# Kernel tuning notes

Measured on AMD Instinct MI355X. Metric: run time of the kernel, lower is better.

## Reference

```python
import jax, jax.numpy as jnp
import numpy as np

B, C, H, W = 2, 512, 64, 64
G = 32  # GroupNorm groups
EPS = 1e-6


def setup_inputs() -> dict:
    key = jax.random.key(0)
    ks = jax.random.split(key, 6)
    s = 1.0 / np.sqrt(C)
    return {
        "x": jax.random.normal(ks[0], (B, C, H, W), dtype=jnp.float32),
        "gn_w": jnp.ones((C,), dtype=jnp.float32),
        "gn_b": jnp.zeros((C,), dtype=jnp.float32),
        "wq": jax.random.normal(ks[1], (C, C), dtype=jnp.float32) * s,
        "bq": jnp.zeros((C,), dtype=jnp.float32),
        "wk": jax.random.normal(ks[2], (C, C), dtype=jnp.float32) * s,
        "bk": jnp.zeros((C,), dtype=jnp.float32),
        "wv": jax.random.normal(ks[3], (C, C), dtype=jnp.float32) * s,
        "bv": jnp.zeros((C,), dtype=jnp.float32),
        "wo": jax.random.normal(ks[4], (C, C), dtype=jnp.float32) * s,
        "bo": jnp.zeros((C,), dtype=jnp.float32),
    }


def _group_norm(x, w, b):
    b_, c_, h_, w_ = x.shape
    xg = x.reshape(b_, G, c_ // G, h_ * w_)
    mu = jnp.mean(xg, axis=(2, 3), keepdims=True)
    var = jnp.var(xg, axis=(2, 3), keepdims=True)
    xn = (xg - mu) * jax.lax.rsqrt(var + EPS)
    xn = xn.reshape(b_, c_, h_ * w_)
    return xn * w[None, :, None] + b[None, :, None]  # [B, C, N]


def reference(x, gn_w, gn_b, wq, bq, wk, bk, wv, bv, wo, bo):
    b, c, h, w = x.shape
    hn = _group_norm(x, gn_w, gn_b)  # [B, C, N]
    # 1x1 convs == per-pixel matmuls over channel dim
    q = jnp.einsum('oc,bcn->bon', wq, hn) + bq[None, :, None]
    k = jnp.einsum('oc,bcn->bon', wk, hn) + bk[None, :, None]
    v = jnp.einsum('oc,bcn->bon', wv, hn) + bv[None, :, None]
    scale = jnp.asarray(c, x.dtype) ** -0.5
    attn = jnp.einsum('bci,bcj->bij', q, k) * scale  # [B, N, N]
    attn = jax.nn.softmax(attn, axis=-1)
    o = jnp.einsum('bij,bcj->bci', attn, v)  # [B, C, N]
    o = jnp.einsum('oc,bcn->bon', wo, o) + bo[None, :, None]
    return x + o.reshape(b, c, h, w)
```

## Files before the change

kernel.cpp:

```cpp
#include <hip/hip_runtime.h>

#define CC 512
#define NPIX 4096
#define NB 2
#define NG 32
#define GSIZE 16
#define EPS 1e-6f

typedef unsigned short u16;
typedef __bf16 bf16x8 __attribute__((ext_vector_type(8)));
typedef float f32x4 __attribute__((ext_vector_type(4)));

__device__ __forceinline__ float bf2f(u16 u) {
  union { unsigned int i; float f; } c; c.i = ((unsigned int)u) << 16; return c.f;
}
__device__ __forceinline__ u16 f2bf(float f) {
  union { float f; unsigned int i; } c; c.f = f;
  unsigned int u = c.i;
  return (u16)((u + 0x7fffu + ((u >> 16) & 1u)) >> 16);
}

__global__ __launch_bounds__(256) void f2bf4x4_kernel(
    const float* __restrict__ s0, const float* __restrict__ s1,
    const float* __restrict__ s2, const float* __restrict__ s3,
    u16* __restrict__ d0, u16* __restrict__ d1,
    u16* __restrict__ d2, u16* __restrict__ d3) {
  const float* s; u16* d;
  switch (blockIdx.y) {
    case 0: s = s0; d = d0; break;
    case 1: s = s1; d = d1; break;
    case 2: s = s2; d = d2; break;
    default: s = s3; d = d3; break;
  }
  int i = blockIdx.x * 256 + threadIdx.x;
  float4 v = ((const float4*)s)[i];
  uint2 pk;
  pk.x = (unsigned)f2bf(v.x) | ((unsigned)f2bf(v.y) << 16);
  pk.y = (unsigned)f2bf(v.z) | ((unsigned)f2bf(v.w) << 16);
  ((uint2*)d)[i] = pk;
}

__global__ __launch_bounds__(256) void concat2_kernel(const float* __restrict__ a,
                                                      const float* __restrict__ b,
                                                      float* __restrict__ o) {
  int i = blockIdx.x * 256 + threadIdx.x;
  o[i] = (i < CC) ? a[i] : b[i - CC];
}

__global__ __launch_bounds__(256) void gn_stats_kernel(const float* __restrict__ x,
                                                       float* __restrict__ stats) {
  int bg = blockIdx.x;
  const float4* p = (const float4*)(x + (long)bg * (GSIZE * NPIX));
  float s = 0.f, ss = 0.f;
  for (int i = threadIdx.x; i < GSIZE * NPIX / 4; i += 256) {
    float4 v = p[i];
    s  += v.x + v.y + v.z + v.w;
    ss += v.x * v.x + v.y * v.y + v.z * v.z + v.w * v.w;
  }
  for (int off = 32; off; off >>= 1) { s += __shfl_xor(s, off); ss += __shfl_xor(ss, off); }
  __shared__ float rs[4], rss[4];
  int wid = threadIdx.x >> 6;
  if ((threadIdx.x & 63) == 0) { rs[wid] = s; rss[wid] = ss; }
  __syncthreads();
  if (threadIdx.x == 0) {
    s = rs[0] + rs[1] + rs[2] + rs[3];
    ss = rss[0] + rss[1] + rss[2] + rss[3];
    float mean = s / (float)(GSIZE * NPIX);
    float var = ss / (float)(GSIZE * NPIX) - mean * mean;
    stats[bg * 2] = mean;
    stats[bg * 2 + 1] = rsqrtf(var + EPS);
  }
}

__global__ __launch_bounds__(256) void gn_apply_kernel(const float* __restrict__ x,
                                                       const float* __restrict__ stats,
                                                       const float* __restrict__ gw,
                                                       const float* __restrict__ gb,
                                                       u16* __restrict__ hn) {
  int n0 = blockIdx.x * 64, c0 = blockIdx.y * 64, b = blockIdx.z;
  __shared__ float tile[64][65];
  int t = threadIdx.x;
  int nj = t & 63, cw = t >> 6;
  #pragma unroll
  for (int r = 0; r < 16; ++r) {
    int ci = cw * 16 + r;
    int c = c0 + ci;
    float mean = stats[(b * NG + (c >> 4)) * 2];
    float rstd = stats[(b * NG + (c >> 4)) * 2 + 1];
    float v = x[((long)b * CC + c) * NPIX + n0 + nj];
    tile[ci][nj] = (v - mean) * rstd * gw[c] + gb[c];
  }
  __syncthreads();
  #pragma unroll
  for (int r = 0; r < 16; ++r) {
    int nn = cw * 16 + r;
    hn[((long)b * NPIX + n0 + nn) * CC + c0 + nj] = f2bf(tile[nj][nn]);
  }
}

__global__ __launch_bounds__(256) void lred_kernel(const float* __restrict__ Lp,
                                                   float* __restrict__ L) {
  int i = blockIdx.x * 256 + threadIdx.x;
  int bz = i / NPIX, row = i % NPIX;
  float s = 0.f;
  #pragma unroll
  for (int b = 0; b < 16; ++b) s += Lp[((long)bz * 16 + b) * NPIX + row];
  L[i] = s;
}

#define BM 128
#define BN 128
#define BKT 64
#define BUFSZ 8192

template<int OUTF32, int BIASMODE, int RESID, int EPI>
__global__ __launch_bounds__(256) void gemm_nt(
    const u16* __restrict__ A, int lda, long aBatch,
    const u16* __restrict__ B, int ldb, long bBatch,
    void* __restrict__ C, int ldc, long cBatch,
    const float* __restrict__ bias,
    const float* __restrict__ resid, long rBatch,
    float* __restrict__ L, int lOff,
    int K, float scale) {
  __shared__ u16 SH[2 * 2 * BUFSZ];
  const int t = threadIdx.x;

  int nwgx = gridDim.x, nwgy = gridDim.y;
  int flat = blockIdx.x + nwgx * (blockIdx.y + nwgy * blockIdx.z);
  int nwg = nwgx * nwgy * gridDim.z;
  int newflat = (flat % 8) * (nwg / 8) + flat / 8;
  const int bx = newflat % nwgx;
  int tmpf = newflat / nwgx;
  const int by = tmpf % nwgy;
  const int bz = tmpf / nwgy;

  const int m0 = by * BM;
  const int n0 = bx * BN;
  const u16* Ab = A + (long)bz * aBatch;
  const u16* Bb = B + (long)bz * bBatch;

  const int lane = t & 63;
  const int wid = t >> 6;
  const int wr = (wid >> 1) * 64;
  const int wc = (wid & 1) * 64;
  const int r16 = lane & 15;
  const int q = lane >> 4;

  const int sRow = wid * 8 + (lane >> 3);
  const int sCol = (((lane & 7) ^ (lane >> 3)) * 8);

  f32x4 acc[4][4] = {};
  const int rsw = r16 & 7;

  const int nt = K / BKT;

  auto stage = [&](int c, int k0) {
    u16* aDst = SH + c * 2 * BUFSZ + wid * 512;
    u16* bDst = SH + c * 2 * BUFSZ + BUFSZ + wid * 512;
    #pragma unroll
    for (int p = 0; p < 4; ++p) {
      __builtin_amdgcn_global_load_lds(
          (const __attribute__((address_space(1))) unsigned int*)(Ab + (long)(m0 + p * 32 + sRow) * lda + k0 + sCol),
          (__attribute__((address_space(3))) unsigned int*)(aDst + p * 2048),
          16, 0, 0);
      __builtin_amdgcn_global_load_lds(
          (const __attribute__((address_space(1))) unsigned int*)(Bb + (long)(n0 + p * 32 + sRow) * ldb + k0 + sCol),
          (__attribute__((address_space(3))) unsigned int*)(bDst + p * 2048),
          16, 0, 0);
    }
  };

  stage(0, 0);

  for (int tt = 0; tt < nt; ++tt) {
    const int pre = tt + 1;
    if (pre < nt) {
      stage(pre & 1, pre * BKT);
      asm volatile("s_waitcnt vmcnt(8)" ::: "memory");
    } else {
      asm volatile("s_waitcnt vmcnt(0)" ::: "memory");
    }
    __builtin_amdgcn_s_barrier();
    __builtin_amdgcn_sched_barrier(0);

    const u16* As_b = SH + (tt & 1) * 2 * BUFSZ;
    const u16* Bs_b = As_b + BUFSZ;
    #pragma unroll
    for (int kk = 0; kk < BKT; kk += 32) {
      bf16x8 af[4], bfr[4];
      const int c0q = (kk >> 3) + q;
      const int colSw = (c0q ^ rsw) * 8;
      #pragma unroll
      for (int i = 0; i < 4; ++i) {
        af[i]  = *(const bf16x8*)&As_b[(wr + i * 16 + r16) * BKT + colSw];
        bfr[i] = *(const bf16x8*)&Bs_b[(wc + i * 16 + r16) * BKT + colSw];
      }
      #pragma unroll
      for (int i = 0; i < 4; ++i)
        #pragma unroll
        for (int j = 0; j < 4; ++j)
          acc[i][j] = __builtin_amdgcn_mfma_f32_16x16x32_bf16(af[i], bfr[j], acc[i][j], 0, 0, 0);
    }
    __builtin_amdgcn_s_barrier();
    __builtin_amdgcn_sched_barrier(0);
  }

  if (EPI == 1) {
    #pragma unroll
    for (int i = 0; i < 4; ++i) {
      #pragma unroll
      for (int r = 0; r < 4; ++r) {
        int row = m0 + wr + i * 16 + q * 4 + r;
        float s = 0.f;
        #pragma unroll
        for (int j = 0; j < 4; ++j) {
          float p = __expf(acc[i][j][r] * scale);
          s += p;
          int col = n0 + wc + j * 16 + r16;
          ((u16*)C)[(long)bz * cBatch + (long)row * ldc + col] = f2bf(p);
        }
        s += __shfl_xor(s, 1); s += __shfl_xor(s, 2);
        s += __shfl_xor(s, 4); s += __shfl_xor(s, 8);
        if (r16 == 0) atomicAdd(&L[(long)bz * NPIX + lOff + row], s);
      }
    }
    return;
  }

  #pragma unroll
  for (int i = 0; i < 4; ++i) {
    #pragma unroll
    for (int r = 0; r < 4; ++r) {
      int row = m0 + wr + i * 16 + q * 4 + r;
      float inv = 1.0f;
      if (EPI == 2) inv = 1.0f / L[(long)bz * NPIX + lOff + row];
      #pragma unroll
      for (int j = 0; j < 4; ++j) {
        int col = n0 + wc + j * 16 + r16;
        float v = acc[i][j][r] * scale;
        if (EPI == 2) v *= inv;
        if (BIASMODE == 1) v += bias[row];
        if (BIASMODE == 2) v += bias[col];
        long off = (long)bz * cBatch + (long)row * ldc + col;
        if (RESID) v += resid[(long)bz * rBatch + (long)row * ldc + col];
        if (OUTF32) ((float*)C)[off] = v;
        else        ((u16*)C)[off] = f2bf(v);
      }
    }
  }
}

__global__ __launch_bounds__(512, 1) void gemm256_exp(
    const u16* __restrict__ A, int lda, long aBatch,
    const u16* __restrict__ B, int ldb, long bBatch,
    u16* __restrict__ C, int ldc, long cBatch,
    float* __restrict__ Lp,
    int K, float scale) {
  __shared__ u16 SH[2][32768];
  const int t = threadIdx.x;

  int nwgx = gridDim.x, nwgy = gridDim.y;
  int flat = blockIdx.x + nwgx * (blockIdx.y + nwgy * blockIdx.z);
  int nwg = nwgx * nwgy * gridDim.z;
  int newflat = (flat % 8) * (nwg / 8) + flat / 8;
  const int bx = newflat % nwgx;
  int tmpf = newflat / nwgx;
  const int by = tmpf % nwgy;
  const int bz = tmpf / nwgy;

  const int m0 = by * 256;
  const int n0 = bx * 256;
  const u16* Ab = A + (long)bz * aBatch;
  const u16* Bb = B + (long)bz * bBatch;
  u16* Cb = C + (long)bz * cBatch;

  const int lane = t & 63;
  const int wid = t >> 6;
  const int wrow = (wid >> 2) * 128;
  const int wcol = (wid & 3) * 64;
  const int r16 = lane & 15;
  const int q = lane >> 4;
  const int rsw = r16 & 7;

  const int sRow = t >> 3;
  const int sCol = ((t & 7) ^ ((t >> 3) & 7)) * 8;

  auto stage = [&](int d, int k0) {
    u16* base = &SH[d][0];
    #pragma unroll
    for (int i = 0; i < 4; ++i)
      __builtin_amdgcn_global_load_lds(
          (const __attribute__((address_space(1))) unsigned int*)(Ab + (long)(m0 + i * 64 + sRow) * lda + k0 + sCol),
          (__attribute__((address_space(3))) unsigned int*)(base + i * 4096 + wid * 512),
          16, 0, 0);
    #pragma unroll
    for (int i = 0; i < 4; ++i)
      __builtin_amdgcn_global_load_lds(
          (const __attribute__((address_space(1))) unsigned int*)(Bb + (long)(n0 + i * 64 + sRow) * ldb + k0 + sCol),
          (__attribute__((address_space(3))) unsigned int*)(base + 16384 + i * 4096 + wid * 512),
          16, 0, 0);
  };

  f32x4 acc[8][4] = {};
  const int nt = K / 64;

  stage(0, 0);

  for (int tt = 0; tt < nt; ++tt) {
    if (tt + 1 < nt) {
      stage((tt + 1) & 1, (tt + 1) * 64);
      asm volatile("s_waitcnt vmcnt(8)" ::: "memory");
    } else {
      asm volatile("s_waitcnt vmcnt(0)" ::: "memory");
    }
    __builtin_amdgcn_s_barrier();

    const u16* As_ = &SH[tt & 1][0];
    const u16* Bs_ = As_ + 16384;
    #pragma unroll
    for (int kk = 0; kk < 2; ++kk) {
      const int cs = ((kk * 4 + q) ^ rsw) * 8;
      bf16x8 af[8], bfv[4];
      #pragma unroll
      for (int i = 0; i < 8; ++i)
        af[i] = *(const bf16x8*)&As_[(wrow + i * 16 + r16) * 64 + cs];
      #pragma unroll
      for (int i = 0; i < 4; ++i)
        bfv[i] = *(const bf16x8*)&Bs_[(wcol + i * 16 + r16) * 64 + cs];
      #pragma unroll
      for (int mi = 0; mi < 8; ++mi)
        #pragma unroll
        for (int ni = 0; ni < 4; ++ni)
          acc[mi][ni] = __builtin_amdgcn_mfma_f32_16x16x32_bf16(af[mi], bfv[ni], acc[mi][ni], 0, 0, 0);
    }
    __builtin_amdgcn_s_barrier();
  }

  float* Lsh = (float*)&SH[0][0];
  #pragma unroll
  for (int mi = 0; mi < 8; ++mi) {
    #pragma unroll
    for (int r = 0; r < 4; ++r) {
      int lrow = mi * 16 + q * 4 + r;
      int row = m0 + wrow + lrow;
      float s = 0.f;
      #pragma unroll
      for (int ni = 0; ni < 4; ++ni) {
        float p = __expf(acc[mi][ni][r] * scale);
        s += p;
        Cb[(long)row * ldc + n0 + wcol + ni * 16 + r16] = f2bf(p);
      }
      s += __shfl_xor(s, 1); s += __shfl_xor(s, 2);
      s += __shfl_xor(s, 4); s += __shfl_xor(s, 8);
      if (r16 == 0) Lsh[((wrow >> 7) * 128 + lrow) * 4 + (wcol >> 6)] = s;
    }
  }
  __syncthreads();
  if (t < 256) {
    const float* lr = &Lsh[t * 4];
    Lp[((long)bz * 16 + bx) * NPIX + m0 + t] = lr[0] + lr[1] + lr[2] + lr[3];
  }
}

extern "C" void kernel_launch(void* const* d_in, const int* in_sizes, int n_in,
                              void* d_out, int out_size, void* d_ws, size_t ws_size,
                              hipStream_t stream) {
  const float* x   = (const float*)d_in[0];
  const float* gnw = (const float*)d_in[1];
  const float* gnb = (const float*)d_in[2];
  const float* wq  = (const float*)d_in[3];
  const float* bq  = (const float*)d_in[4];
  const float* wk  = (const float*)d_in[5];
  const float* bk_ = (const float*)d_in[6];
  const float* wv  = (const float*)d_in[7];
  const float* bv  = (const float*)d_in[8];
  const float* wo  = (const float*)d_in[9];
  const float* bo  = (const float*)d_in[10];
  float* out = (float*)d_out;

  char* wsp = (char*)d_ws;
  auto alloc = [&](size_t bytes) {
    char* r = wsp; wsp += (bytes + 255) & ~(size_t)255; return r;
  };
  u16* wqb = (u16*)alloc((size_t)CC * CC * 2);
  u16* wkb = (u16*)alloc((size_t)CC * CC * 2);
  u16* wvb = (u16*)alloc((size_t)CC * CC * 2);
  u16* wob = (u16*)alloc((size_t)CC * CC * 2);
  float* bqk = (float*)alloc((size_t)2 * CC * 4);
  float* stats = (float*)alloc((size_t)NB * NG * 2 * 4);
  float* lsum = (float*)alloc((size_t)NB * NPIX * 4);
  float* lpart = (float*)alloc((size_t)NB * 16 * NPIX * 4);
  u16* hn  = (u16*)alloc((size_t)NB * NPIX * CC * 2);
  u16* qkt = (u16*)alloc((size_t)NB * NPIX * (2 * CC) * 2);
  u16* vcn = (u16*)alloc((size_t)NB * CC * NPIX * 2);
  u16* ot  = (u16*)alloc((size_t)NB * NPIX * CC * 2);
  size_t used = (size_t)(wsp - (char*)d_ws);
  size_t rem = ws_size > used ? ws_size - used : 0;
  int CH = 256;
  if ((size_t)NB * 1024 * NPIX * 2 <= rem) CH = 1024;
  if ((size_t)NB * 4096 * NPIX * 2 <= rem) CH = 4096;
  u16* SP = (u16*)alloc((size_t)NB * CH * NPIX * 2);

  dim3 blk(256);
  f2bf4x4_kernel<<<dim3(CC * CC / 1024, 4), blk, 0, stream>>>(
      wq, wk, wv, wo, wqb, wkb, wvb, wob);
  concat2_kernel<<<2 * CC / 256, blk, 0, stream>>>(bq, bk_, bqk);
  hipMemsetAsync(lsum, 0, (size_t)NB * NPIX * 4, stream);

  gn_stats_kernel<<<NB * NG, blk, 0, stream>>>(x, stats);
  gn_apply_kernel<<<dim3(NPIX / 64, CC / 64, NB), blk, 0, stream>>>(x, stats, gnw, gnb, hn);

  gemm_nt<0, 2, 0, 0><<<dim3(2 * CC / BN, NPIX / BM, NB), blk, 0, stream>>>(
      hn, CC, (long)NPIX * CC, wqb, CC, 0, qkt, 2 * CC, (long)NPIX * 2 * CC,
      bqk, nullptr, 0, nullptr, 0, CC, 1.0f);
  gemm_nt<0, 1, 0, 0><<<dim3(NPIX / BN, CC / BM, NB), blk, 0, stream>>>(
      wvb, CC, 0, hn, CC, (long)NPIX * CC, vcn, NPIX, (long)CC * NPIX,
      bv, nullptr, 0, nullptr, 0, CC, 1.0f);

  const u16* qt = qkt;
  const u16* kt = qkt + CC;
  const float scale = 0.044194173824159216f;
  for (int i0 = 0; i0 < NPIX; i0 += CH) {
    if (CH == 4096) {
      gemm256_exp<<<dim3(NPIX / 256, NPIX / 256, NB), dim3(512), 0, stream>>>(
          qt, 2 * CC, (long)NPIX * 2 * CC, kt, 2 * CC, (long)NPIX * 2 * CC,
          SP, NPIX, (long)CH * NPIX, lpart, CC, scale);
      lred_kernel<<<NB * NPIX / 256, blk, 0, stream>>>(lpart, lsum);
    } else {
      gemm_nt<0, 0, 0, 1><<<dim3(NPIX / BN, CH / BM, NB), blk, 0, stream>>>(
          qt + (long)i0 * 2 * CC, 2 * CC, (long)NPIX * 2 * CC, kt, 2 * CC, (long)NPIX * 2 * CC,
          SP, NPIX, (long)CH * NPIX, nullptr, nullptr, 0, lsum, i0, CC, scale);
    }
    gemm_nt<0, 0, 0, 2><<<dim3(CC / BN, CH / BM, NB), blk, 0, stream>>>(
        SP, NPIX, (long)CH * NPIX, vcn, NPIX, (long)CC * NPIX,
        ot + (long)i0 * CC, CC, (long)NPIX * CC, nullptr, nullptr, 0, lsum, i0, NPIX, 1.0f);
  }

  gemm_nt<1, 1, 1, 0><<<dim3(NPIX / BN, CC / BM, NB), blk, 0, stream>>>(
      wob, CC, 0, ot, CC, (long)NPIX * CC, out, NPIX, (long)CC * NPIX,
      bo, x, (long)CC * NPIX, nullptr, 0, CC, 1.0f);
}
```

Before: 166.0 us.

## Triple-buffer QK^T exp GEMM with K=32 tiles and interleaved prefetch

Reworks the gemm256_exp main loop from a double-buffered K=64 tile to a triple-buffered K=32 tile with a prefetch distance of two. Global-to-LDS loads for the tile two steps ahead are split into halves and issued between LDS fragment reads and MFMA bursts. Priority raising is added around the MFMA blocks. The aim is to hide global load latency and LDS waits behind matrix work. In exchange there are more loop iterations and barriers, a new swizzle pattern for the narrower tile, and tighter vmcnt accounting that must match the number of loads in flight.

```diff
diff --git a/kernel.cpp b/kernel.cpp
--- a/kernel.cpp
+++ b/kernel.cpp
@@ -250,13 +250,16 @@
   }
 }
 
+#define BK3 32
+#define TBUF 8192
+
 __global__ __launch_bounds__(512, 1) void gemm256_exp(
     const u16* __restrict__ A, int lda, long aBatch,
     const u16* __restrict__ B, int ldb, long bBatch,
     u16* __restrict__ C, int ldc, long cBatch,
     float* __restrict__ Lp,
     int K, float scale) {
-  __shared__ u16 SH[2][32768];
+  __shared__ u16 SH[3][2 * TBUF];
   const int t = threadIdx.x;
 
   int nwgx = gridDim.x, nwgy = gridDim.y;
@@ -280,62 +283,79 @@
   const int wcol = (wid & 3) * 64;
   const int r16 = lane & 15;
   const int q = lane >> 4;
-  const int rsw = r16 & 7;
-
-  const int sRow = t >> 3;
-  const int sCol = ((t & 7) ^ ((t >> 3) & 7)) * 8;
-
-  auto stage = [&](int d, int k0) {
-    u16* base = &SH[d][0];
-    #pragma unroll
-    for (int i = 0; i < 4; ++i)
-      __builtin_amdgcn_global_load_lds(
-          (const __attribute__((address_space(1))) unsigned int*)(Ab + (long)(m0 + i * 64 + sRow) * lda + k0 + sCol),
-          (__attribute__((address_space(3))) unsigned int*)(base + i * 4096 + wid * 512),
-          16, 0, 0);
-    #pragma unroll
-    for (int i = 0; i < 4; ++i)
-      __builtin_amdgcn_global_load_lds(
-          (const __attribute__((address_space(1))) unsigned int*)(Bb + (long)(n0 + i * 64 + sRow) * ldb + k0 + sCol),
-          (__attribute__((address_space(3))) unsigned int*)(base + 16384 + i * 4096 + wid * 512),
-          16, 0, 0);
+
+  const int sRow = t >> 2;
+  const int sCol = ((t & 3) ^ ((t >> 3) & 3)) * 8;
+
+  auto stageHalf = [&](int buf, int k0, int op, int half) {
+    const u16* src = (op ? Bb + (long)(n0 + half * 128 + sRow) * ldb
+                         : Ab + (long)(m0 + half * 128 + sRow) * lda) + k0 + sCol;
+    u16* dst = &SH[buf][op * TBUF + half * 4096 + wid * 512];
+    __builtin_amdgcn_global_load_lds(
+        (const __attribute__((address_space(1))) unsigned int*)src,
+        (__attribute__((address_space(3))) unsigned int*)dst, 16, 0, 0);
   };
+  auto stageTile = [&](int buf, int k0) {
+    stageHalf(buf, k0, 0, 0); stageHalf(buf, k0, 1, 0);
+    stageHalf(buf, k0, 0, 1); stageHalf(buf, k0, 1, 1);
+  };
 
   f32x4 acc[8][4] = {};
-  const int nt = K / 64;
-
-  stage(0, 0);
+  const int nt = K / BK3;
+  const int cs = (q ^ ((r16 >> 1) & 3)) * 8;
+
+  stageTile(0, 0);
+  stageTile(1, BK3);
 
   for (int tt = 0; tt < nt; ++tt) {
     if (tt + 1 < nt) {
-      stage((tt + 1) & 1, (tt + 1) * 64);
-      asm volatile("s_waitcnt vmcnt(8)" ::: "memory");
+      asm volatile("s_waitcnt vmcnt(4)" ::: "memory");
     } else {
       asm volatile("s_waitcnt vmcnt(0)" ::: "memory");
     }
     __builtin_amdgcn_s_barrier();
-
-    const u16* As_ = &SH[tt & 1][0];
-    const u16* Bs_ = As_ + 16384;
-    #pragma unroll
-    for (int kk = 0; kk < 2; ++kk) {
-      const int cs = ((kk * 4 + q) ^ rsw) * 8;
-      bf16x8 af[8], bfv[4];
-      #pragma unroll
-      for (int i = 0; i < 8; ++i)
-        af[i] = *(const bf16x8*)&As_[(wrow + i * 16 + r16) * 64 + cs];
-      #pragma unroll
-      for (int i = 0; i < 4; ++i)
-        bfv[i] = *(const bf16x8*)&Bs_[(wcol + i * 16 + r16) * 64 + cs];
-      #pragma unroll
-      for (int mi = 0; mi < 8; ++mi)
-        #pragma unroll
-        for (int ni = 0; ni < 4; ++ni)
-          acc[mi][ni] = __builtin_amdgcn_mfma_f32_16x16x32_bf16(af[mi], bfv[ni], acc[mi][ni], 0, 0, 0);
-    }
+    __builtin_amdgcn_sched_barrier(0);
+
+    const u16* As_ = &SH[tt % 3][0];
+    const u16* Bs_ = As_ + TBUF;
+    const int pre = tt + 2;
+
+    bf16x8 a1[4], bfv[4];
+    #pragma unroll
+    for (int i = 0; i < 4; ++i)
+      a1[i] = *(const bf16x8*)&As_[(wrow + i * 16 + r16) * BK3 + cs];
+    #pragma unroll
+    for (int i = 0; i < 4; ++i)
+      bfv[i] = *(const bf16x8*)&Bs_[(wcol + i * 16 + r16) * BK3 + cs];
+    if (pre < nt) { stageHalf(pre % 3, pre * BK3, 0, 0); stageHalf(pre % 3, pre * BK3, 1, 0); }
+    asm volatile("s_waitcnt lgkmcnt(0)" ::: "memory");
+    __builtin_amdgcn_sched_barrier(0);
+    __builtin_amdgcn_s_setprio(1);
+    #pragma unroll
+    for (int mi = 0; mi < 4; ++mi)
+      #pragma unroll
+      for (int ni = 0; ni < 4; ++ni)
+        acc[mi][ni] = __builtin_amdgcn_mfma_f32_16x16x32_bf16(a1[mi], bfv[ni], acc[mi][ni], 0, 0, 0);
+    __builtin_amdgcn_s_setprio(0);
     __builtin_amdgcn_s_barrier();
-  }
-
+
+    bf16x8 a2[4];
+    #pragma unroll
+    for (int i = 0; i < 4; ++i)
+      a2[i] = *(const bf16x8*)&As_[(wrow + (4 + i) * 16 + r16) * BK3 + cs];
+    if (pre < nt) { stageHalf(pre % 3, pre * BK3, 0, 1); stageHalf(pre % 3, pre * BK3, 1, 1); }
+    asm volatile("s_waitcnt lgkmcnt(0)" ::: "memory");
+    __builtin_amdgcn_sched_barrier(0);
+    __builtin_amdgcn_s_setprio(1);
+    #pragma unroll
+    for (int mi = 0; mi < 4; ++mi)
+      #pragma unroll
+      for (int ni = 0; ni < 4; ++ni)
+        acc[4 + mi][ni] = __builtin_amdgcn_mfma_f32_16x16x32_bf16(a2[mi], bfv[ni], acc[4 + mi][ni], 0, 0, 0);
+    __builtin_amdgcn_s_setprio(0);
+  }
+
+  __builtin_amdgcn_s_barrier();
   float* Lsh = (float*)&SH[0][0];
   #pragma unroll
   for (int mi = 0; mi < 8; ++mi) {
```

New measurement: 170.8 us. 1.03x slower.

## Fold Wq^T·Wk and Wo·Wv into combined weights to drop projection GEMMs

Applied to the files above, without the earlier changes.

Precomputes Wq^T·Wk and Wo·Wv as bf16 matrices with a small batched GEMM. The score GEMM then uses hn directly against hn·(Wq^T Wk), and the PV GEMM writes the final output with softmax normalisation, folded bias and residual in a new epilogue. The bk term is dropped because it is constant along each softmax row, and the bq contribution becomes a per-key column bias added inside the exp. This removes the Q projection and the output-projection GEMM plus the ot intermediate, at the cost of small transpose, weight-product and bias kernels, and extra bf16 rounding from the precomposed weights.

```diff
diff --git a/kernel.cpp b/kernel.cpp
--- a/kernel.cpp
+++ b/kernel.cpp
@@ -20,18 +20,8 @@
   return (u16)((u + 0x7fffu + ((u >> 16) & 1u)) >> 16);
 }
 
-__global__ __launch_bounds__(256) void f2bf4x4_kernel(
-    const float* __restrict__ s0, const float* __restrict__ s1,
-    const float* __restrict__ s2, const float* __restrict__ s3,
-    u16* __restrict__ d0, u16* __restrict__ d1,
-    u16* __restrict__ d2, u16* __restrict__ d3) {
-  const float* s; u16* d;
-  switch (blockIdx.y) {
-    case 0: s = s0; d = d0; break;
-    case 1: s = s1; d = d1; break;
-    case 2: s = s2; d = d2; break;
-    default: s = s3; d = d3; break;
-  }
+__global__ __launch_bounds__(256) void f2bf1_kernel(const float* __restrict__ s,
+                                                    u16* __restrict__ d) {
   int i = blockIdx.x * 256 + threadIdx.x;
   float4 v = ((const float4*)s)[i];
   uint2 pk;
@@ -40,11 +30,74 @@
   ((uint2*)d)[i] = pk;
 }
 
-__global__ __launch_bounds__(256) void concat2_kernel(const float* __restrict__ a,
-                                                      const float* __restrict__ b,
-                                                      float* __restrict__ o) {
+__global__ __launch_bounds__(256) void f2bfT_kernel(
+    const float* __restrict__ s0, const float* __restrict__ s1,
+    const float* __restrict__ s2,
+    u16* __restrict__ d0, u16* __restrict__ d1, u16* __restrict__ d2) {
+  const float* s; u16* d;
+  switch (blockIdx.z) {
+    case 0: s = s0; d = d0; break;
+    case 1: s = s1; d = d1; break;
+    default: s = s2; d = d2; break;
+  }
+  __shared__ float tile[64][65];
+  int a0 = blockIdx.x * 64, b0 = blockIdx.y * 64;
+  int tx = threadIdx.x & 63, w = threadIdx.x >> 6;
+  #pragma unroll
+  for (int r = 0; r < 16; ++r) {
+    int row = w * 16 + r;
+    tile[row][tx] = s[(long)(b0 + row) * CC + a0 + tx];
+  }
+  __syncthreads();
+  #pragma unroll
+  for (int r = 0; r < 16; ++r) {
+    int row = w * 16 + r;
+    d[(long)(a0 + row) * CC + b0 + tx] = f2bf(tile[tx][row]);
+  }
+}
+
+__global__ __launch_bounds__(256) void ubias_kernel(const u16* __restrict__ wkT,
+                                                    const float* __restrict__ bq,
+                                                    float* __restrict__ u) {
+  int b = blockIdx.x * 256 + threadIdx.x;
+  const u16* row = wkT + (long)b * CC;
+  float s = 0.f;
+  for (int c = 0; c < CC; c += 8) {
+    uint4 raw = *(const uint4*)(row + c);
+    const u16* pr = (const u16*)&raw;
+    #pragma unroll
+    for (int k = 0; k < 8; ++k) s += bf2f(pr[k]) * bq[c + k];
+  }
+  u[b] = s;
+}
+
+__global__ __launch_bounds__(256) void wobv_kernel(const float* __restrict__ wo,
+                                                   const float* __restrict__ bv,
+                                                   const float* __restrict__ bo,
+                                                   float* __restrict__ wobv) {
+  int o = blockIdx.x * 256 + threadIdx.x;
+  const float* row = wo + (long)o * CC;
+  float s = bo[o];
+  for (int c = 0; c < CC; c += 4) {
+    float4 v = *(const float4*)(row + c);
+    s += v.x * bv[c] + v.y * bv[c + 1] + v.z * bv[c + 2] + v.w * bv[c + 3];
+  }
+  wobv[o] = s;
+}
+
+__global__ __launch_bounds__(256) void cb_kernel(const u16* __restrict__ hn,
+                                                 const float* __restrict__ u,
+                                                 float* __restrict__ cb, float scale) {
   int i = blockIdx.x * 256 + threadIdx.x;
-  o[i] = (i < CC) ? a[i] : b[i - CC];
+  const u16* row = hn + (long)i * CC;
+  float s = 0.f;
+  for (int c = 0; c < CC; c += 8) {
+    uint4 raw = *(const uint4*)(row + c);
+    const u16* pr = (const u16*)&raw;
+    #pragma unroll
+    for (int k = 0; k < 8; ++k) s += bf2f(pr[k]) * u[c + k];
+  }
+  cb[i] = s * scale;
 }
 
 __global__ __launch_bounds__(256) void gn_stats_kernel(const float* __restrict__ x,
@@ -121,6 +174,7 @@
     const float* __restrict__ bias,
     const float* __restrict__ resid, long rBatch,
     float* __restrict__ L, int lOff,
+    const float* __restrict__ cbias,
     int K, float scale) {
   __shared__ u16 SH[2 * 2 * BUFSZ];
   const int t = threadIdx.x;
@@ -206,6 +260,10 @@
   }
 
   if (EPI == 1) {
+    float cbv[4];
+    #pragma unroll
+    for (int j = 0; j < 4; ++j)
+      cbv[j] = cbias[(long)bz * NPIX + n0 + wc + j * 16 + r16];
     #pragma unroll
     for (int i = 0; i < 4; ++i) {
       #pragma unroll
@@ -214,7 +272,7 @@
         float s = 0.f;
         #pragma unroll
         for (int j = 0; j < 4; ++j) {
-          float p = __expf(acc[i][j][r] * scale);
+          float p = __expf(acc[i][j][r] * scale + cbv[j]);
           s += p;
           int col = n0 + wc + j * 16 + r16;
           ((u16*)C)[(long)bz * cBatch + (long)row * ldc + col] = f2bf(p);
@@ -227,18 +285,38 @@
     return;
   }
 
+  if (EPI == 3) {
+    float invc[4];
+    #pragma unroll
+    for (int j = 0; j < 4; ++j)
+      invc[j] = 1.0f / L[(long)bz * NPIX + lOff + n0 + wc + j * 16 + r16];
+    #pragma unroll
+    for (int i = 0; i < 4; ++i) {
+      #pragma unroll
+      for (int r = 0; r < 4; ++r) {
+        int row = m0 + wr + i * 16 + q * 4 + r;
+        float bia = bias[row];
+        #pragma unroll
+        for (int j = 0; j < 4; ++j) {
+          int col = n0 + wc + j * 16 + r16;
+          long off = (long)bz * cBatch + (long)row * ldc + col;
+          ((float*)C)[off] = acc[i][j][r] * invc[j] + bia +
+                             resid[(long)bz * rBatch + (long)row * ldc + col];
+        }
+      }
+    }
+    return;
+  }
+
   #pragma unroll
   for (int i = 0; i < 4; ++i) {
     #pragma unroll
     for (int r = 0; r < 4; ++r) {
       int row = m0 + wr + i * 16 + q * 4 + r;
-      float inv = 1.0f;
-      if (EPI == 2) inv = 1.0f / L[(long)bz * NPIX + lOff + row];
       #pragma unroll
       for (int j = 0; j < 4; ++j) {
         int col = n0 + wc + j * 16 + r16;
         float v = acc[i][j][r] * scale;
-        if (EPI == 2) v *= inv;
         if (BIASMODE == 1) v += bias[row];
         if (BIASMODE == 2) v += bias[col];
         long off = (long)bz * cBatch + (long)row * ldc + col;
@@ -254,7 +332,7 @@
     const u16* __restrict__ A, int lda, long aBatch,
     const u16* __restrict__ B, int ldb, long bBatch,
     u16* __restrict__ C, int ldc, long cBatch,
-    float* __restrict__ Lp,
+    float* __restrict__ Lp, const float* __restrict__ cb,
     int K, float scale) {
   __shared__ u16 SH[2][32768];
   const int t = threadIdx.x;
@@ -336,6 +414,10 @@
     __builtin_amdgcn_s_barrier();
   }
 
+  float cbv[4];
+  #pragma unroll
+  for (int ni = 0; ni < 4; ++ni)
+    cbv[ni] = cb[(long)bz * NPIX + n0 + wcol + ni * 16 + r16];
   float* Lsh = (float*)&SH[0][0];
   #pragma unroll
   for (int mi = 0; mi < 8; ++mi) {
@@ -346,7 +428,7 @@
       float s = 0.f;
       #pragma unroll
       for (int ni = 0; ni < 4; ++ni) {
-        float p = __expf(acc[mi][ni][r] * scale);
+        float p = __expf(acc[mi][ni][r] * scale + cbv[ni]);
         s += p;
         Cb[(long)row * ldc + n0 + wcol + ni * 16 + r16] = f2bf(p);
       }
@@ -377,23 +459,25 @@
   const float* wo  = (const float*)d_in[9];
   const float* bo  = (const float*)d_in[10];
   float* out = (float*)d_out;
+  (void)bk_;
 
   char* wsp = (char*)d_ws;
   auto alloc = [&](size_t bytes) {
     char* r = wsp; wsp += (bytes + 255) & ~(size_t)255; return r;
   };
-  u16* wqb = (u16*)alloc((size_t)CC * CC * 2);
-  u16* wkb = (u16*)alloc((size_t)CC * CC * 2);
-  u16* wvb = (u16*)alloc((size_t)CC * CC * 2);
-  u16* wob = (u16*)alloc((size_t)CC * CC * 2);
-  float* bqk = (float*)alloc((size_t)2 * CC * 4);
+  const size_t WSZ = (size_t)CC * CC;
+  u16* wA = (u16*)alloc(2 * WSZ * 2);
+  u16* wB = (u16*)alloc(2 * WSZ * 2);
+  u16* wC = (u16*)alloc(2 * WSZ * 2);
+  float* ub    = (float*)alloc(CC * 4);
+  float* wobv  = (float*)alloc(CC * 4);
+  float* cb    = (float*)alloc((size_t)NB * NPIX * 4);
   float* stats = (float*)alloc((size_t)NB * NG * 2 * 4);
-  float* lsum = (float*)alloc((size_t)NB * NPIX * 4);
+  float* lsum  = (float*)alloc((size_t)NB * NPIX * 4);
   float* lpart = (float*)alloc((size_t)NB * 16 * NPIX * 4);
   u16* hn  = (u16*)alloc((size_t)NB * NPIX * CC * 2);
-  u16* qkt = (u16*)alloc((size_t)NB * NPIX * (2 * CC) * 2);
-  u16* vcn = (u16*)alloc((size_t)NB * CC * NPIX * 2);
-  u16* ot  = (u16*)alloc((size_t)NB * NPIX * CC * 2);
+  u16* k2  = (u16*)alloc((size_t)NB * NPIX * CC * 2);
+  u16* von = (u16*)alloc((size_t)NB * CC * NPIX * 2);
   size_t used = (size_t)(wsp - (char*)d_ws);
   size_t rem = ws_size > used ? ws_size - used : 0;
   int CH = 256;
@@ -402,41 +486,43 @@
   u16* SP = (u16*)alloc((size_t)NB * CH * NPIX * 2);
 
   dim3 blk(256);
-  f2bf4x4_kernel<<<dim3(CC * CC / 1024, 4), blk, 0, stream>>>(
-      wq, wk, wv, wo, wqb, wkb, wvb, wob);
-  concat2_kernel<<<2 * CC / 256, blk, 0, stream>>>(bq, bk_, bqk);
+  const float scale = 0.044194173824159216f;
+
+  f2bfT_kernel<<<dim3(8, 8, 3), blk, 0, stream>>>(wq, wk, wv, wA, wB, wB + WSZ);
+  f2bf1_kernel<<<CC * CC / 1024, blk, 0, stream>>>(wo, wA + WSZ);
+  ubias_kernel<<<CC / 256, blk, 0, stream>>>(wB, bq, ub);
+  wobv_kernel<<<CC / 256, blk, 0, stream>>>(wo, bv, bo, wobv);
   hipMemsetAsync(lsum, 0, (size_t)NB * NPIX * 4, stream);
+
+  gemm_nt<0, 0, 0, 0><<<dim3(CC / BN, CC / BM, 2), blk, 0, stream>>>(
+      wA, CC, (long)WSZ, wB, CC, (long)WSZ, wC, CC, (long)WSZ,
+      nullptr, nullptr, 0, nullptr, 0, nullptr, CC, 1.0f);
 
   gn_stats_kernel<<<NB * NG, blk, 0, stream>>>(x, stats);
   gn_apply_kernel<<<dim3(NPIX / 64, CC / 64, NB), blk, 0, stream>>>(x, stats, gnw, gnb, hn);
-
-  gemm_nt<0, 2, 0, 0><<<dim3(2 * CC / BN, NPIX / BM, NB), blk, 0, stream>>>(
-      hn, CC, (long)NPIX * CC, wqb, CC, 0, qkt, 2 * CC, (long)NPIX * 2 * CC,
-      bqk, nullptr, 0, nullptr, 0, CC, 1.0f);
-  gemm_nt<0, 1, 0, 0><<<dim3(NPIX / BN, CC / BM, NB), blk, 0, stream>>>(
-      wvb, CC, 0, hn, CC, (long)NPIX * CC, vcn, NPIX, (long)CC * NPIX,
-      bv, nullptr, 0, nullptr, 0, CC, 1.0f);
-
-  const u16* qt = qkt;
-  const u16* kt = qkt + CC;
-  const float scale = 0.044194173824159216f;
+  cb_kernel<<<NB * NPIX / 256, blk, 0, stream>>>(hn, ub, cb, scale);
+
+  gemm_nt<0, 0, 0, 0><<<dim3(CC / BN, NPIX / BM, NB), blk, 0, stream>>>(
+      hn, CC, (long)NPIX * CC, wC, CC, 0, k2, CC, (long)NPIX * CC,
+      nullptr, nullptr, 0, nullptr, 0, nullptr, CC, 1.0f);
+  gemm_nt<0, 0, 0, 0><<<dim3(NPIX / BN, CC / BM, NB), blk, 0, stream>>>(
+      wC + WSZ, CC, 0, hn, CC, (long)NPIX * CC, von, NPIX, (long)CC * NPIX,
+      nullptr, nullptr, 0, nullptr, 0, nullptr, CC, 1.0f);
+
   for (int i0 = 0; i0 < NPIX; i0 += CH) {
     if (CH == 4096) {
       gemm256_exp<<<dim3(NPIX / 256, NPIX / 256, NB), dim3(512), 0, stream>>>(
-          qt, 2 * CC, (long)NPIX * 2 * CC, kt, 2 * CC, (long)NPIX * 2 * CC,
-          SP, NPIX, (long)CH * NPIX, lpart, CC, scale);
+          hn, CC, (long)NPIX * CC, k2, CC, (long)NPIX * CC,
+          SP, NPIX, (long)CH * NPIX, lpart, cb, CC, scale);
       lred_kernel<<<NB * NPIX / 256, blk, 0, stream>>>(lpart, lsum);
     } else {
       gemm_nt<0, 0, 0, 1><<<dim3(NPIX / BN, CH / BM, NB), blk, 0, stream>>>(
-          qt + (long)i0 * 2 * CC, 2 * CC, (long)NPIX * 2 * CC, kt, 2 * CC, (long)NPIX * 2 * CC,
-          SP, NPIX, (long)CH * NPIX, nullptr, nullptr, 0, lsum, i0, CC, scale);
-    }
-    gemm_nt<0, 0, 0, 2><<<dim3(CC / BN, CH / BM, NB), blk, 0, stream>>>(
-        SP, NPIX, (long)CH * NPIX, vcn, NPIX, (long)CC * NPIX,
-        ot + (long)i0 * CC, CC, (long)NPIX * CC, nullptr, nullptr, 0, lsum, i0, NPIX, 1.0f);
-  }
-
-  gemm_nt<1, 1, 1, 0><<<dim3(NPIX / BN, CC / BM, NB), blk, 0, stream>>>(
-      wob, CC, 0, ot, CC, (long)NPIX * CC, out, NPIX, (long)CC * NPIX,
-      bo, x, (long)CC * NPIX, nullptr, 0, CC, 1.0f);
-}
+          hn + (long)i0 * CC, CC, (long)NPIX * CC, k2, CC, (long)NPIX * CC,
+          SP, NPIX, (long)CH * NPIX, nullptr, nullptr, 0, lsum, i0, cb, CC, scale);
+    }
+    gemm_nt<1, 1, 1, 3><<<dim3(CH / BN, CC / BM, NB), blk, 0, stream>>>(
+        von, NPIX, (long)CC * NPIX, SP, NPIX, (long)CH * NPIX,
+        out + i0, NPIX, (long)CC * NPIX, wobv, x + i0, (long)CC * NPIX,
+        lsum, i0, nullptr, NPIX, 1.0f);
+  }
+}
```

Measured after the change: 201.9 us. +21.6%, slower.
